# Kernel optimization log

Hardware: AMD Instinct MI355X
Metric: run time of the kernel (lower is better)

Reference implementation:

```python
import jax, jax.numpy as jnp
import numpy as np

N_NODES = 50000
N_EDGES = 800000
IN_DIM = 128
OUT_DIM = 64


def setup_inputs() -> dict:
    key = jax.random.key(0)
    k_x, k_r, k_c, k_v, k_w = jax.random.split(key, 5)
    x = jax.random.normal(k_x, (N_NODES, IN_DIM), dtype=jnp.float32)
    edge_row = jax.random.randint(k_r, (N_EDGES,), 0, N_NODES, dtype=jnp.int64)
    edge_col = jax.random.randint(k_c, (N_EDGES,), 0, N_NODES, dtype=jnp.int64)
    edge_val = jax.random.uniform(k_v, (N_EDGES,), dtype=jnp.float32)
    # kaiming_uniform-style init: bound = sqrt(6 / fan_in) with a=sqrt(5) gain folded in torch;
    # exact init values don't affect correctness testing, use a uniform of similar scale.
    bound = float(np.sqrt(6.0 / IN_DIM))
    weight = jax.random.uniform(k_w, (IN_DIM, OUT_DIM), dtype=jnp.float32,
                                minval=-bound, maxval=bound)
    return {"x": x, "edge_row": edge_row, "edge_col": edge_col,
            "edge_val": edge_val, "weight": weight}


def reference(x, edge_row, edge_col, edge_val, weight):
    # dropout p=0.0 -> identity (module default)
    support = x @ weight                              # [N, out_dim] dense GEMM
    # spmm(adj, support): out[i] = sum_e adj_val[e] * support[col[e]] for row[e]==i
    messages = edge_val[:, None] * support[edge_col]  # [E, out_dim] gather
    out = jax.ops.segment_sum(messages, edge_row, num_segments=N_NODES)  # scatter-add
    return jax.nn.relu(out)
```

## Files before the change

kernel.cpp:

```cpp
#include <hip/hip_runtime.h>

#define N_NODES 50000
#define N_EDGES 800000
#define IN_DIM 128
#define OUT_DIM 64

#define GROUP_SHIFT 6
#define GROUP_ROWS 64
#define N_GROUPS 782
#define SLAB 1216
#define CHUNK2 2048
#define FILL_BLOCKS 391

typedef _Float16 h2 __attribute__((ext_vector_type(2)));
typedef _Float16 h4 __attribute__((ext_vector_type(4)));
typedef _Float16 h8 __attribute__((ext_vector_type(8)));
typedef float    f4 __attribute__((ext_vector_type(4)));

#define LDK 136

__global__ __launch_bounds__(256) void fused_gemm_fill(const float* __restrict__ x,
                                                       const float* __restrict__ w,
                                                       const int* __restrict__ erow,
                                                       const int* __restrict__ ecol,
                                                       const float* __restrict__ eval,
                                                       _Float16* __restrict__ support,
                                                       int* __restrict__ gcursor,
                                                       int2* __restrict__ bucket) {
    __shared__ char smem[GROUP_ROWS * LDK * 2 + OUT_DIM * LDK * 2];
    const int tid = threadIdx.x;

    if (blockIdx.x >= FILL_BLOCKS) {
        _Float16* xb = (_Float16*)smem;
        _Float16* wt = (_Float16*)(smem + GROUP_ROWS * LDK * 2);

        {
            const int n_s = tid >> 2;
            const int kp0 = tid & 3;
            #pragma unroll
            for (int it = 0; it < 16; ++it) {
                int kp = kp0 + (it << 2);
                int k  = kp << 1;
                h2 hv = { (_Float16)w[(size_t)k * OUT_DIM + n_s],
                          (_Float16)w[(size_t)(k + 1) * OUT_DIM + n_s] };
                *(h2*)&wt[n_s * LDK + k] = hv;
            }
        }
        const int rowbase = (blockIdx.x - FILL_BLOCKS) * GROUP_ROWS;
        for (int i = tid; i < GROUP_ROWS * (IN_DIM / 4); i += 256) {
            int r  = i >> 5;
            int kq = i & 31;
            int row = rowbase + r;
            float4 v = (row < N_NODES)
                           ? *(const float4*)&x[(size_t)row * IN_DIM + kq * 4]
                           : make_float4(0.f, 0.f, 0.f, 0.f);
            h4 hv = { (_Float16)v.x, (_Float16)v.y, (_Float16)v.z, (_Float16)v.w };
            *(h4*)&xb[r * LDK + kq * 4] = hv;
        }
        __syncthreads();

        const int wave = tid >> 6;
        const int lane = tid & 63;
        const int mrow = lane & 15;
        const int quad = lane >> 4;
        const int m0   = wave * 16;

        f4 acc[4];
        #pragma unroll
        for (int t = 0; t < 4; ++t) acc[t] = (f4){0.f, 0.f, 0.f, 0.f};

        #pragma unroll
        for (int ks = 0; ks < 4; ++ks) {
            int kof = ks * 32 + quad * 8;
            h8 a = *(h8*)&xb[(m0 + mrow) * LDK + kof];
            #pragma unroll
            for (int t = 0; t < 4; ++t) {
                h8 b = *(h8*)&wt[(t * 16 + mrow) * LDK + kof];
                acc[t] = __builtin_amdgcn_mfma_f32_16x16x32_f16(a, b, acc[t], 0, 0, 0);
            }
        }

        #pragma unroll
        for (int t = 0; t < 4; ++t) {
            #pragma unroll
            for (int r = 0; r < 4; ++r) {
                int row = rowbase + m0 + quad * 4 + r;
                if (row < N_NODES)
                    support[(size_t)row * OUT_DIM + t * 16 + mrow] = (_Float16)acc[t][r];
            }
        }
    } else {
        int* lcnt  = (int*)smem;
        int* lbase = lcnt + N_GROUPS;
        for (int i = tid; i < N_GROUPS; i += 256) lcnt[i] = 0;
        __syncthreads();
        const int base = blockIdx.x * CHUNK2;
        #pragma unroll 4
        for (int i = 0; i < CHUNK2 / 256; ++i) {
            int e = base + tid + i * 256;
            if (e < N_EDGES) atomicAdd(&lcnt[erow[e] >> GROUP_SHIFT], 1);
        }
        __syncthreads();
        for (int i = tid; i < N_GROUPS; i += 256) {
            int c = lcnt[i];
            lbase[i] = c ? atomicAdd(&gcursor[i], c) : 0;
            lcnt[i]  = 0;
        }
        __syncthreads();
        #pragma unroll 4
        for (int i = 0; i < CHUNK2 / 256; ++i) {
            int e = base + tid + i * 256;
            if (e < N_EDGES) {
                int r = erow[e];
                int g = r >> GROUP_SHIFT;
                int p = atomicAdd(&lcnt[g], 1);
                bucket[(size_t)g * SLAB + lbase[g] + p] =
                    make_int2(((r & (GROUP_ROWS - 1)) << 16) | ecol[e],
                              __float_as_int(eval[e]));
            }
        }
    }
}

__global__ __launch_bounds__(1024) void reduce_group(const int* __restrict__ gcursor,
                                                     const int2* __restrict__ bucket,
                                                     const _Float16* __restrict__ support,
                                                     float* __restrict__ out) {
    __shared__ int2 ebuf[SLAB];
    __shared__ int2 ebuf2[SLAB];
    __shared__ int  rcnt[GROUP_ROWS];
    __shared__ int  rstart[GROUP_ROWS + 1];
    __shared__ int  rcur[GROUP_ROWS];
    const int grp = blockIdx.x;
    const int cnt = min(gcursor[grp], SLAB);
    const size_t sb = (size_t)grp * SLAB;
    const int tid = threadIdx.x;

    if (tid < GROUP_ROWS) rcnt[tid] = 0;
    __syncthreads();
    for (int j = tid; j < cnt; j += 1024) {
        int2 cv = bucket[sb + j];
        ebuf[j] = cv;
        atomicAdd(&rcnt[cv.x >> 16], 1);
    }
    __syncthreads();
    if (tid < GROUP_ROWS) {
        int v = rcnt[tid];
        int s = v;
        #pragma unroll
        for (int off = 1; off < 64; off <<= 1) {
            int t = __shfl_up(s, off, 64);
            if (tid >= off) s += t;
        }
        rstart[tid] = s - v;
        rcur[tid]   = s - v;
        if (tid == 63) rstart[64] = s;
    }
    __syncthreads();
    for (int j = tid; j < cnt; j += 1024) {
        int2 cv = ebuf[j];
        int rl = cv.x >> 16;
        int p  = atomicAdd(&rcur[rl], 1);
        ebuf2[p] = cv;
    }
    __syncthreads();

    const int g  = tid & 15;
    const int lr = tid >> 4;
    const int row = grp * GROUP_ROWS + lr;
    const int jb = rstart[lr];
    const int je = rstart[lr + 1];
    float4 acc0 = make_float4(0.f, 0.f, 0.f, 0.f);
    float4 acc1 = make_float4(0.f, 0.f, 0.f, 0.f);
    int j = jb;
    for (; j + 1 < je; j += 2) {
        int2 cv0 = ebuf2[j];
        int2 cv1 = ebuf2[j + 1];
        float v0 = __int_as_float(cv0.y);
        float v1 = __int_as_float(cv1.y);
        h4 s0 = *(const h4*)&support[(size_t)(cv0.x & 0xFFFF) * OUT_DIM + g * 4];
        h4 s1 = *(const h4*)&support[(size_t)(cv1.x & 0xFFFF) * OUT_DIM + g * 4];
        acc0.x += v0 * (float)s0[0];
        acc0.y += v0 * (float)s0[1];
        acc0.z += v0 * (float)s0[2];
        acc0.w += v0 * (float)s0[3];
        acc1.x += v1 * (float)s1[0];
        acc1.y += v1 * (float)s1[1];
        acc1.z += v1 * (float)s1[2];
        acc1.w += v1 * (float)s1[3];
    }
    if (j < je) {
        int2 cv = ebuf2[j];
        float v = __int_as_float(cv.y);
        h4 sr = *(const h4*)&support[(size_t)(cv.x & 0xFFFF) * OUT_DIM + g * 4];
        acc0.x += v * (float)sr[0];
        acc0.y += v * (float)sr[1];
        acc0.z += v * (float)sr[2];
        acc0.w += v * (float)sr[3];
    }
    if (row < N_NODES) {
        float4 a;
        a.x = fmaxf(acc0.x + acc1.x, 0.f);
        a.y = fmaxf(acc0.y + acc1.y, 0.f);
        a.z = fmaxf(acc0.z + acc1.z, 0.f);
        a.w = fmaxf(acc0.w + acc1.w, 0.f);
        *(float4*)&out[(size_t)row * OUT_DIM + g * 4] = a;
    }
}

extern "C" void kernel_launch(void* const* d_in, const int* in_sizes, int n_in,
                              void* d_out, int out_size, void* d_ws, size_t ws_size,
                              hipStream_t stream) {
    const float* x    = (const float*)d_in[0];
    const int*   erow = (const int*)  d_in[1];
    const int*   ecol = (const int*)  d_in[2];
    const float* ev   = (const float*)d_in[3];
    const float* w    = (const float*)d_in[4];
    float* out = (float*)d_out;

    char* ws = (char*)d_ws;
    _Float16* support = (_Float16*)ws;
    int*  gcursor = (int*)(ws + 6400000);
    int2* bucket  = (int2*)(ws + 6403200);

    hipMemsetAsync(gcursor, 0, sizeof(int) * N_GROUPS, stream);

    fused_gemm_fill<<<FILL_BLOCKS + N_GROUPS, 256, 0, stream>>>(
        x, w, erow, ecol, ev, support, gcursor, bucket);

    reduce_group<<<N_GROUPS, 1024, 0, stream>>>(gcursor, bucket, support, out);
}
```

Before: 124.3 us.

## Replace per-row counting sort with shared-memory float atomics in group reduce

The reduce kernel no longer counts, prefix-sums and scatters edges by local row before the gather. Each 16-thread group now takes one edge at a time, gathers the support slice and atomically adds the scaled values into a 64x64 shared-memory accumulator, prefetching the next bucket entry. This removes several barriers and the two staging buffers, and drops the block size to 512 threads. In exchange it relies on LDS float atomics, which can contend when edges share a row, and the summation order becomes nondeterministic.

```diff
diff --git a/kernel.cpp b/kernel.cpp
--- a/kernel.cpp
+++ b/kernel.cpp
@@ -122,89 +122,59 @@
     }
 }
 
-__global__ __launch_bounds__(1024) void reduce_group(const int* __restrict__ gcursor,
-                                                     const int2* __restrict__ bucket,
-                                                     const _Float16* __restrict__ support,
-                                                     float* __restrict__ out) {
-    __shared__ int2 ebuf[SLAB];
-    __shared__ int2 ebuf2[SLAB];
-    __shared__ int  rcnt[GROUP_ROWS];
-    __shared__ int  rstart[GROUP_ROWS + 1];
-    __shared__ int  rcur[GROUP_ROWS];
+__global__ __launch_bounds__(512) void reduce_group(const int* __restrict__ gcursor,
+                                                    const int2* __restrict__ bucket,
+                                                    const _Float16* __restrict__ support,
+                                                    float* __restrict__ out) {
+    __shared__ float accum[GROUP_ROWS][OUT_DIM];
     const int grp = blockIdx.x;
     const int cnt = min(gcursor[grp], SLAB);
     const size_t sb = (size_t)grp * SLAB;
     const int tid = threadIdx.x;
 
-    if (tid < GROUP_ROWS) rcnt[tid] = 0;
+    {
+        float4* az = (float4*)&accum[0][0];
+        const float4 z = make_float4(0.f, 0.f, 0.f, 0.f);
+        az[tid] = z;
+        az[tid + 512] = z;
+    }
     __syncthreads();
-    for (int j = tid; j < cnt; j += 1024) {
-        int2 cv = bucket[sb + j];
-        ebuf[j] = cv;
-        atomicAdd(&rcnt[cv.x >> 16], 1);
+
+    const int u = tid >> 4;
+    const int g = tid & 15;
+
+    int j = u;
+    int2 cv = (j < cnt) ? bucket[sb + j] : make_int2(0, 0);
+    while (j < cnt) {
+        const int jn = j + 32;
+        int2 nx = (jn < cnt) ? bucket[sb + jn] : make_int2(0, 0);
+        const int   rl = cv.x >> 16;
+        const float v  = __int_as_float(cv.y);
+        h4 s = *(const h4*)&support[(size_t)(cv.x & 0xFFFF) * OUT_DIM + g * 4];
+        float* a = &accum[rl][g * 4];
+        atomicAdd(a + 0, v * (float)s[0]);
+        atomicAdd(a + 1, v * (float)s[1]);
+        atomicAdd(a + 2, v * (float)s[2]);
+        atomicAdd(a + 3, v * (float)s[3]);
+        cv = nx;
+        j = jn;
     }
     __syncthreads();
-    if (tid < GROUP_ROWS) {
-        int v = rcnt[tid];
-        int s = v;
-        #pragma unroll
-        for (int off = 1; off < 64; off <<= 1) {
-            int t = __shfl_up(s, off, 64);
-            if (tid >= off) s += t;
-        }
-        rstart[tid] = s - v;
-        rcur[tid]   = s - v;
-        if (tid == 63) rstart[64] = s;
-    }
-    __syncthreads();
-    for (int j = tid; j < cnt; j += 1024) {
-        int2 cv = ebuf[j];
-        int rl = cv.x >> 16;
-        int p  = atomicAdd(&rcur[rl], 1);
-        ebuf2[p] = cv;
-    }
-    __syncthreads();
-
-    const int g  = tid & 15;
-    const int lr = tid >> 4;
-    const int row = grp * GROUP_ROWS + lr;
-    const int jb = rstart[lr];
-    const int je = rstart[lr + 1];
-    float4 acc0 = make_float4(0.f, 0.f, 0.f, 0.f);
-    float4 acc1 = make_float4(0.f, 0.f, 0.f, 0.f);
-    int j = jb;
-    for (; j + 1 < je; j += 2) {
-        int2 cv0 = ebuf2[j];
-        int2 cv1 = ebuf2[j + 1];
-        float v0 = __int_as_float(cv0.y);
-        float v1 = __int_as_float(cv1.y);
-        h4 s0 = *(const h4*)&support[(size_t)(cv0.x & 0xFFFF) * OUT_DIM + g * 4];
-        h4 s1 = *(const h4*)&support[(size_t)(cv1.x & 0xFFFF) * OUT_DIM + g * 4];
-        acc0.x += v0 * (float)s0[0];
-        acc0.y += v0 * (float)s0[1];
-        acc0.z += v0 * (float)s0[2];
-        acc0.w += v0 * (float)s0[3];
-        acc1.x += v1 * (float)s1[0];
-        acc1.y += v1 * (float)s1[1];
-        acc1.z += v1 * (float)s1[2];
-        acc1.w += v1 * (float)s1[3];
-    }
-    if (j < je) {
-        int2 cv = ebuf2[j];
-        float v = __int_as_float(cv.y);
-        h4 sr = *(const h4*)&support[(size_t)(cv.x & 0xFFFF) * OUT_DIM + g * 4];
-        acc0.x += v * (float)sr[0];
-        acc0.y += v * (float)sr[1];
-        acc0.z += v * (float)sr[2];
-        acc0.w += v * (float)sr[3];
-    }
-    if (row < N_NODES) {
-        float4 a;
-        a.x = fmaxf(acc0.x + acc1.x, 0.f);
-        a.y = fmaxf(acc0.y + acc1.y, 0.f);
-        a.z = fmaxf(acc0.z + acc1.z, 0.f);
-        a.w = fmaxf(acc0.w + acc1.w, 0.f);
-        *(float4*)&out[(size_t)row * OUT_DIM + g * 4] = a;
+
+    #pragma unroll
+    for (int i = tid; i < GROUP_ROWS * (OUT_DIM / 4); i += 512) {
+        const int lr = i >> 4;
+        const int q  = i & 15;
+        const int row = grp * GROUP_ROWS + lr;
+        if (row < N_NODES) {
+            const float* a = &accum[lr][q * 4];
+            float4 r;
+            r.x = fmaxf(a[0], 0.f);
+            r.y = fmaxf(a[1], 0.f);
+            r.z = fmaxf(a[2], 0.f);
+            r.w = fmaxf(a[3], 0.f);
+            *(float4*)&out[(size_t)row * OUT_DIM + q * 4] = r;
+        }
     }
 }
 
@@ -228,5 +198,5 @@
     fused_gemm_fill<<<FILL_BLOCKS + N_GROUPS, 256, 0, stream>>>(
         x, w, erow, ecol, ev, support, gcursor, bucket);
 
-    reduce_group<<<N_GROUPS, 1024, 0, stream>>>(gcursor, bucket, support, out);
+    reduce_group<<<N_GROUPS, 512, 0, stream>>>(gcursor, bucket, support, out);
 }
```

Measured after the change: 444.7 us. 3.58x slower.

## Replace global atomic bucket cursors with cooperative-kernel count, scan and deterministic fill

Applied to the files above, without the earlier changes.

Turns the per-block global atomicAdd cursor allocation into a three-phase count/prefix-scan/fill scheme, run as one cooperative kernel with grid-wide syncs. GEMM work is folded into the same blocks after the fill, and the memset is dropped. A three-launch fallback covers the case where the cooperative launch fails. The aim is to remove global atomic contention and the memset, at the cost of two grid barriers, extra count and offset arrays, and 1024 resident blocks of 256 threads at up to 4 blocks per CU.

```diff
diff --git a/kernel.cpp b/kernel.cpp
--- a/kernel.cpp
+++ b/kernel.cpp
@@ -1,4 +1,7 @@
 #include <hip/hip_runtime.h>
+#include <hip/hip_cooperative_groups.h>
+
+namespace cg = cooperative_groups;
 
 #define N_NODES 50000
 #define N_EDGES 800000
@@ -9,8 +12,10 @@
 #define GROUP_ROWS 64
 #define N_GROUPS 782
 #define SLAB 1216
-#define CHUNK2 2048
-#define FILL_BLOCKS 391
+#define GRID_B 1024
+#define CHUNK 800
+#define NCH 1000
+#define GEMM_FALLBACK_BASE 1000
 
 typedef _Float16 h2 __attribute__((ext_vector_type(2)));
 typedef _Float16 h4 __attribute__((ext_vector_type(4)));
@@ -19,18 +24,107 @@
 
 #define LDK 136
 
-__global__ __launch_bounds__(256) void fused_gemm_fill(const float* __restrict__ x,
-                                                       const float* __restrict__ w,
-                                                       const int* __restrict__ erow,
-                                                       const int* __restrict__ ecol,
-                                                       const float* __restrict__ eval,
-                                                       _Float16* __restrict__ support,
-                                                       int* __restrict__ gcursor,
-                                                       int2* __restrict__ bucket) {
+__global__ __launch_bounds__(256, 4) void fused_all(const float* __restrict__ x,
+                                                    const float* __restrict__ w,
+                                                    const int* __restrict__ erow,
+                                                    const int* __restrict__ ecol,
+                                                    const float* __restrict__ eval,
+                                                    _Float16* __restrict__ support,
+                                                    unsigned short* __restrict__ cnt16,
+                                                    unsigned short* __restrict__ rbase,
+                                                    int* __restrict__ gtot,
+                                                    int2* __restrict__ bucket,
+                                                    int phase) {
     __shared__ char smem[GROUP_ROWS * LDK * 2 + OUT_DIM * LDK * 2];
     const int tid = threadIdx.x;
-
-    if (blockIdx.x >= FILL_BLOCKS) {
+    const int bid = blockIdx.x;
+    const bool coop = (phase == 3);
+
+    if (coop || phase == 0) {
+        if (bid < NCH) {
+            int* lcnt = (int*)smem;
+            for (int i = tid; i < N_GROUPS; i += 256) lcnt[i] = 0;
+            __syncthreads();
+            const int base = bid * CHUNK;
+            for (int i = tid; i < CHUNK; i += 256)
+                atomicAdd(&lcnt[erow[base + i] >> GROUP_SHIFT], 1);
+            __syncthreads();
+            for (int i = tid; i < N_GROUPS; i += 256)
+                cnt16[(size_t)bid * N_GROUPS + i] = (unsigned short)lcnt[i];
+        }
+        if (!coop) return;
+        cg::this_grid().sync();
+    }
+
+    if (coop || phase == 1) {
+        if (bid < N_GROUPS) {
+            const int g = bid;
+            int s[4];
+            int lsum = 0;
+            #pragma unroll
+            for (int k = 0; k < 4; ++k) {
+                int ch = tid * 4 + k;
+                s[k] = (ch < NCH) ? (int)cnt16[(size_t)ch * N_GROUPS + g] : 0;
+                lsum += s[k];
+            }
+            const int lane = tid & 63;
+            const int wid  = tid >> 6;
+            int incl = lsum;
+            #pragma unroll
+            for (int off = 1; off < 64; off <<= 1) {
+                int t = __shfl_up(incl, off, 64);
+                if (lane >= off) incl += t;
+            }
+            int* wsum = (int*)smem;
+            if (lane == 63) wsum[wid] = incl;
+            __syncthreads();
+            int wo = 0;
+            #pragma unroll
+            for (int wv = 0; wv < 4; ++wv)
+                if (wv < wid) wo += wsum[wv];
+            int run = wo + incl - lsum;
+            #pragma unroll
+            for (int k = 0; k < 4; ++k) {
+                int ch = tid * 4 + k;
+                if (ch < NCH) {
+                    rbase[(size_t)ch * N_GROUPS + g] = (unsigned short)run;
+                    run += s[k];
+                }
+            }
+            if (tid == 255) gtot[g] = wo + incl;
+        }
+        if (!coop) return;
+        cg::this_grid().sync();
+    }
+
+    const int fill_ch = bid;
+    const int gemm_grp = coop ? bid : bid - GEMM_FALLBACK_BASE;
+    const bool do_fill = (fill_ch < NCH);
+    const bool do_gemm = coop ? (bid < N_GROUPS)
+                              : (bid >= GEMM_FALLBACK_BASE &&
+                                 gemm_grp < N_GROUPS);
+
+    if (do_fill) {
+        int* lcnt = (int*)smem;
+        for (int i = tid; i < N_GROUPS; i += 256) lcnt[i] = 0;
+        __syncthreads();
+        const unsigned short* rb = &rbase[(size_t)fill_ch * N_GROUPS];
+        const int base = fill_ch * CHUNK;
+        for (int i = tid; i < CHUNK; i += 256) {
+            int e = base + i;
+            int r = erow[e];
+            int g = r >> GROUP_SHIFT;
+            int p = atomicAdd(&lcnt[g], 1);
+            int pos = (int)rb[g] + p;
+            if (pos < SLAB)
+                bucket[(size_t)g * SLAB + pos] =
+                    make_int2(((r & (GROUP_ROWS - 1)) << 16) | ecol[e],
+                              __float_as_int(eval[e]));
+        }
+        __syncthreads();
+    }
+
+    if (do_gemm) {
         _Float16* xb = (_Float16*)smem;
         _Float16* wt = (_Float16*)(smem + GROUP_ROWS * LDK * 2);
 
@@ -46,7 +140,7 @@
                 *(h2*)&wt[n_s * LDK + k] = hv;
             }
         }
-        const int rowbase = (blockIdx.x - FILL_BLOCKS) * GROUP_ROWS;
+        const int rowbase = gemm_grp * GROUP_ROWS;
         for (int i = tid; i < GROUP_ROWS * (IN_DIM / 4); i += 256) {
             int r  = i >> 5;
             int kq = i & 31;
@@ -89,40 +183,10 @@
                     support[(size_t)row * OUT_DIM + t * 16 + mrow] = (_Float16)acc[t][r];
             }
         }
-    } else {
-        int* lcnt  = (int*)smem;
-        int* lbase = lcnt + N_GROUPS;
-        for (int i = tid; i < N_GROUPS; i += 256) lcnt[i] = 0;
-        __syncthreads();
-        const int base = blockIdx.x * CHUNK2;
-        #pragma unroll 4
-        for (int i = 0; i < CHUNK2 / 256; ++i) {
-            int e = base + tid + i * 256;
-            if (e < N_EDGES) atomicAdd(&lcnt[erow[e] >> GROUP_SHIFT], 1);
-        }
-        __syncthreads();
-        for (int i = tid; i < N_GROUPS; i += 256) {
-            int c = lcnt[i];
-            lbase[i] = c ? atomicAdd(&gcursor[i], c) : 0;
-            lcnt[i]  = 0;
-        }
-        __syncthreads();
-        #pragma unroll 4
-        for (int i = 0; i < CHUNK2 / 256; ++i) {
-            int e = base + tid + i * 256;
-            if (e < N_EDGES) {
-                int r = erow[e];
-                int g = r >> GROUP_SHIFT;
-                int p = atomicAdd(&lcnt[g], 1);
-                bucket[(size_t)g * SLAB + lbase[g] + p] =
-                    make_int2(((r & (GROUP_ROWS - 1)) << 16) | ecol[e],
-                              __float_as_int(eval[e]));
-            }
-        }
     }
 }
 
-__global__ __launch_bounds__(1024) void reduce_group(const int* __restrict__ gcursor,
+__global__ __launch_bounds__(1024) void reduce_group(const int* __restrict__ gtot,
                                                      const int2* __restrict__ bucket,
                                                      const _Float16* __restrict__ support,
                                                      float* __restrict__ out) {
@@ -132,7 +196,7 @@
     __shared__ int  rstart[GROUP_ROWS + 1];
     __shared__ int  rcur[GROUP_ROWS];
     const int grp = blockIdx.x;
-    const int cnt = min(gcursor[grp], SLAB);
+    const int cnt = min(gtot[grp], SLAB);
     const size_t sb = (size_t)grp * SLAB;
     const int tid = threadIdx.x;
 
@@ -219,14 +283,27 @@
     float* out = (float*)d_out;
 
     char* ws = (char*)d_ws;
-    _Float16* support = (_Float16*)ws;
-    int*  gcursor = (int*)(ws + 6400000);
-    int2* bucket  = (int2*)(ws + 6403200);
-
-    hipMemsetAsync(gcursor, 0, sizeof(int) * N_GROUPS, stream);
-
-    fused_gemm_fill<<<FILL_BLOCKS + N_GROUPS, 256, 0, stream>>>(
-        x, w, erow, ecol, ev, support, gcursor, bucket);
-
-    reduce_group<<<N_GROUPS, 1024, 0, stream>>>(gcursor, bucket, support, out);
+    _Float16*       support = (_Float16*)ws;
+    unsigned short* cnt16   = (unsigned short*)(ws + 6400000);
+    unsigned short* rbase   = (unsigned short*)(ws + 7964000);
+    int*            gtot    = (int*)(ws + 9528000);
+    int2*           bucket  = (int2*)(ws + 9531136);
+
+    int phase = 3;
+    void* args[] = { (void*)&x, (void*)&w, (void*)&erow, (void*)&ecol,
+                     (void*)&ev, (void*)&support, (void*)&cnt16, (void*)&rbase,
+                     (void*)&gtot, (void*)&bucket, (void*)&phase };
+    hipError_t cerr = hipLaunchCooperativeKernel((const void*)fused_all,
+                                                 dim3(GRID_B), dim3(256),
+                                                 args, 0, stream);
+    if (cerr != hipSuccess) {
+        fused_all<<<NCH, 256, 0, stream>>>(x, w, erow, ecol, ev, support,
+                                           cnt16, rbase, gtot, bucket, 0);
+        fused_all<<<N_GROUPS, 256, 0, stream>>>(x, w, erow, ecol, ev, support,
+                                                cnt16, rbase, gtot, bucket, 1);
+        fused_all<<<GEMM_FALLBACK_BASE + N_GROUPS, 256, 0, stream>>>(
+            x, w, erow, ecol, ev, support, cnt16, rbase, gtot, bucket, 2);
+    }
+
+    reduce_group<<<N_GROUPS, 1024, 0, stream>>>(gtot, bucket, support, out);
 }
```

Result: slower. 385.0 us (+209.7%).
